# Performance work log

Measured on AMD Instinct MI355X. Metric: run time of the kernel, lower is better.

Reference implementation:

```python
import math
import jax, jax.numpy as jnp
import numpy as np

KV_RANK = 512
NOPE = 128
ROPE = 64
V_DIM = 128
N_HEADS = 16
DIM = 2048
EPS = 1e-6
# qk_head_dim = 192; max_seq_len > original_seq_len -> mscale correction
_MSCALE = 0.1 * 1.0 * math.log(40.0) + 1.0
SOFTMAX_SCALE = (NOPE + ROPE) ** -0.5 * _MSCALE * _MSCALE


def _rmsnorm(x, w):
    y = x * jax.lax.rsqrt(jnp.mean(x * x, axis=-1, keepdims=True) + EPS)
    return y * w


def _rope(x, cos, sin):
    # x: [b, s, h, d] with d even; pairs are interleaved (complex view semantics)
    xr, xi = x[..., 0::2], x[..., 1::2]
    c = cos[None, :, None, :]
    s = sin[None, :, None, :]
    yr = xr * c - xi * s
    yi = xr * s + xi * c
    return jnp.stack([yr, yi], axis=-1).reshape(x.shape)


def setup_inputs() -> dict:
    key = jax.random.key(0)
    ks = jax.random.split(key, 6)
    B, S = 2, 2048
    x = jax.random.normal(ks[0], (B, S, DIM), dtype=jnp.float32)
    # standard RoPE angles: pos * inv_freq, theta=10000
    inv_freq = 1.0 / (10000.0 ** (np.arange(0, ROPE, 2, dtype=np.float32) / ROPE))
    angles = jnp.asarray(np.arange(S, dtype=np.float32)[:, None] * inv_freq[None, :])
    wq = jax.random.normal(ks[1], (N_HEADS * (NOPE + ROPE), DIM), dtype=jnp.float32) * (DIM ** -0.5)
    wkv_a = jax.random.normal(ks[2], (KV_RANK + ROPE, DIM), dtype=jnp.float32) * (DIM ** -0.5)
    wkv_b = jax.random.normal(ks[3], (N_HEADS * (NOPE + V_DIM), KV_RANK), dtype=jnp.float32) * (KV_RANK ** -0.5)
    wo = jax.random.normal(ks[4], (DIM, N_HEADS * V_DIM), dtype=jnp.float32) * ((N_HEADS * V_DIM) ** -0.5)
    kv_norm_w = jnp.ones((KV_RANK,), dtype=jnp.float32)
    return {"x": x, "angles": angles, "wq": wq, "wkv_a": wkv_a,
            "wkv_b": wkv_b, "wo": wo, "kv_norm_w": kv_norm_w}


def reference(x, angles, wq, wkv_a, wkv_b, wo, kv_norm_w):
    B, S, _ = x.shape
    cos, sin = jnp.cos(angles), jnp.sin(angles)  # [S, ROPE//2]

    # query projection
    q = (x @ wq.T).reshape(B, S, N_HEADS, NOPE + ROPE)
    q_nope, q_pe = q[..., :NOPE], q[..., NOPE:]
    q_pe = _rope(q_pe, cos, sin)

    # low-rank kv projection
    kv = x @ wkv_a.T  # [B, S, KV_RANK + ROPE]
    kv_c, k_pe = kv[..., :KV_RANK], kv[..., KV_RANK:]
    k_pe = _rope(k_pe[:, :, None, :], cos, sin)[:, :, 0]  # [B, S, ROPE]
    c = _rmsnorm(kv_c, kv_norm_w)  # latent kv cache [B, S, KV_RANK]

    # weight absorption: fold W^UK into q
    wkv_b_h = wkv_b.reshape(N_HEADS, NOPE + V_DIM, KV_RANK)
    q_abs = jnp.einsum('bshd,hdc->bshc', q_nope, wkv_b_h[:, :NOPE])

    scores = (jnp.einsum('bshc,btc->bsht', q_abs, c)
              + jnp.einsum('bshr,btr->bsht', q_pe, k_pe)) * SOFTMAX_SCALE

    # causal mask (prefill, start_pos=0)
    mask = jnp.where(jnp.tril(jnp.ones((S, S), dtype=bool)), 0.0, -jnp.inf)
    scores = scores + mask[None, :, None, :]
    probs = jax.nn.softmax(scores.astype(jnp.float32), axis=-1).astype(x.dtype)

    o_lat = jnp.einsum('bsht,btc->bshc', probs, c)
    o = jnp.einsum('bshc,hdc->bshd', o_lat, wkv_b_h[:, NOPE:])  # [B,S,H,V]
    return o.reshape(B, S, N_HEADS * V_DIM) @ wo.T
```

## Files before the change

### kernel.cpp

```cpp
#include <hip/hip_runtime.h>
#include <hip/hip_bf16.h>

typedef unsigned short u16;
typedef unsigned int   u32;
typedef __attribute__((ext_vector_type(8))) short bf16x8;
typedef __attribute__((ext_vector_type(4))) float f32x4;

#define NH   16
#define SS   2048

__device__ __forceinline__ u16 bf16b(float f) {
  union { float f; u32 u; } v; v.f = f;
  u32 r = (v.u + 0x7fffu + ((v.u >> 16) & 1u)) >> 16;
  return (u16)r;
}
__device__ __forceinline__ float bf2f(u16 v) {
  union { u32 u; float f; } x; x.u = (u32)v << 16; return x.f;
}
__device__ __forceinline__ f32x4 mfma16(bf16x8 a, bf16x8 b, f32x4 c) {
  return __builtin_amdgcn_mfma_f32_16x16x32_bf16(a, b, c, 0, 0, 0);
}
__device__ __forceinline__ void gl_lds16(const u16* g, u16* l) {
  __builtin_amdgcn_global_load_lds(
      (const __attribute__((address_space(1))) void*)g,
      (__attribute__((address_space(3))) void*)l, 16, 0, 0);
}

__global__ __launch_bounds__(256) void zerok(float* __restrict__ p, long n)
{
  long i = ((long)blockIdx.x * 256 + threadIdx.x) * 4;
  if (i < n) { p[i] = 0.f; p[i+1] = 0.f; p[i+2] = 0.f; p[i+3] = 0.f; }
}

__global__ __launch_bounds__(256) void castk(const float* __restrict__ src,
                                             u16* __restrict__ dst, long n)
{
  long i = ((long)blockIdx.x * 256 + threadIdx.x) * 4;
  if (i >= n) return;
  const float4 f = *(const float4*)(src + i);
  uint2 v;
  v.x = (u32)bf16b(f.x) | ((u32)bf16b(f.y) << 16);
  v.y = (u32)bf16b(f.z) | ((u32)bf16b(f.w) << 16);
  *(uint2*)(dst + i) = v;
}

__global__ __launch_bounds__(256) void wsplit(const float* __restrict__ wb,
                                              u16* __restrict__ T1, u16* __restrict__ Wv)
{
  const long i = (long)blockIdx.x * 256 + threadIdx.x;
  const int h   = (int)(i >> 16);
  const int rem = (int)(i & 65535);
  { const int c = rem >> 7, d = rem & 127;
    T1[i] = bf16b(wb[((long)(h * 256 + d)) * 512 + c]); }
  { const int d = rem >> 9, c = rem & 511;
    Wv[i] = bf16b(wb[((long)(h * 256 + 128 + d)) * 512 + c]); }
}

template<int OUTBF>
__global__ __launch_bounds__(256, 2)
void gemm_bt(const u16* __restrict__ A, const u16* __restrict__ W, void* __restrict__ Cout,
             int M, int N, int K, int lda, int ldw, int ldc,
             long aStride, long wStride, long cStride)
{
  __shared__ u16 As[128 * 40];
  __shared__ u16 Bs[128 * 40];
  const int tid = threadIdx.x;
  const int wave = tid >> 6, lane = tid & 63, g = lane >> 4, l15 = lane & 15;
  const int z = blockIdx.z;
  A += (long)z * aStride;  W += (long)z * wStride;
  const long cOff = (long)z * cStride;
  const int m0 = blockIdx.y * 128, n0 = blockIdx.x * 128;
  const int mq = (wave >> 1) * 64, nq = (wave & 1) * 64;
  const int srow = tid >> 1, scol = (tid & 1) * 16;

  const f32x4 fzero = {0.f, 0.f, 0.f, 0.f};
  f32x4 acc[4][4];
#pragma unroll
  for (int i = 0; i < 4; i++)
#pragma unroll
    for (int j = 0; j < 4; j++) acc[i][j] = fzero;

  for (int k0 = 0; k0 < K; k0 += 32) {
    const u16* aSrc = A + (long)(m0 + srow) * lda + k0 + scol;
    uint4 av0 = *(const uint4*)aSrc;
    uint4 av1 = *(const uint4*)(aSrc + 8);
    uint4 bv0 = make_uint4(0, 0, 0, 0), bv1 = make_uint4(0, 0, 0, 0);
    if (n0 + srow < N) {
      const u16* wSrc = W + (long)(n0 + srow) * ldw + k0 + scol;
      bv0 = *(const uint4*)wSrc;
      bv1 = *(const uint4*)(wSrc + 8);
    }
    __syncthreads();
    *(uint4*)&As[srow * 40 + scol]     = av0;
    *(uint4*)&As[srow * 40 + scol + 8] = av1;
    *(uint4*)&Bs[srow * 40 + scol]     = bv0;
    *(uint4*)&Bs[srow * 40 + scol + 8] = bv1;
    __syncthreads();

    bf16x8 af[4], bfr[4];
#pragma unroll
    for (int i = 0; i < 4; i++) af[i]  = *(const bf16x8*)&As[(mq + i * 16 + l15) * 40 + g * 8];
#pragma unroll
    for (int j = 0; j < 4; j++) bfr[j] = *(const bf16x8*)&Bs[(nq + j * 16 + l15) * 40 + g * 8];
#pragma unroll
    for (int i = 0; i < 4; i++)
#pragma unroll
      for (int j = 0; j < 4; j++)
        acc[i][j] = mfma16(af[i], bfr[j], acc[i][j]);
  }

#pragma unroll
  for (int i = 0; i < 4; i++) {
    const int r0 = m0 + mq + i * 16 + g * 4;
#pragma unroll
    for (int j = 0; j < 4; j++) {
      const int c = n0 + nq + j * 16 + l15;
      if (c < N) {
#pragma unroll
        for (int r = 0; r < 4; r++) {
          const long idx = cOff + (long)(r0 + r) * ldc + c;
          if (OUTBF) ((u16*)Cout)[idx]   = bf16b(acc[i][j][r]);
          else       ((float*)Cout)[idx] = acc[i][j][r];
        }
      }
    }
  }
}

__global__ __launch_bounds__(256) void qpack(const u16* __restrict__ q,
                                             const float* __restrict__ angles,
                                             u16* __restrict__ qpe)
{
  const int s = blockIdx.x;
  const int sseq = s & (SS - 1);
  const int tid = threadIdx.x;
#pragma unroll
  for (int pp = 0; pp < 2; pp++) {
    const int p = tid * 2 + pp;
    const int h = p >> 5, j = p & 31;
    const float xr = bf2f(q[(long)s * 3072 + h * 192 + 128 + 2 * j]);
    const float xi = bf2f(q[(long)s * 3072 + h * 192 + 128 + 2 * j + 1]);
    float sn, cs;
    __sincosf(angles[sseq * 32 + j], &sn, &cs);
    const u32 pk = (u32)bf16b(xr * cs - xi * sn) | ((u32)bf16b(xr * sn + xi * cs) << 16);
    *(u32*)(qpe + ((long)s * NH + h) * 64 + 2 * j) = pk;
  }
}

__global__ __launch_bounds__(256) void kvpack(const u16* __restrict__ kv,
                                              const float* __restrict__ angles,
                                              const float* __restrict__ kvw,
                                              u16* __restrict__ cb, u16* __restrict__ kpe)
{
  const int row = blockIdx.x * 4 + (threadIdx.x >> 6);
  const int lane = threadIdx.x & 63;
  const int sseq = row & (SS - 1);
  const u16* src = kv + (long)row * 576;
  float v[8]; float ss = 0.f;
#pragma unroll
  for (int j = 0; j < 8; j++) { float t = bf2f(src[lane + j * 64]); v[j] = t; ss += t * t; }
#pragma unroll
  for (int d = 1; d < 64; d <<= 1) ss += __shfl_xor(ss, d, 64);
  const float rn = 1.0f / sqrtf(ss * (1.f / 512.f) + 1e-6f);
#pragma unroll
  for (int j = 0; j < 8; j++)
    cb[(long)row * 512 + lane + j * 64] = bf16b(v[j] * rn * kvw[lane + j * 64]);
  if (lane < 32) {
    const float xr = bf2f(src[512 + 2 * lane]), xi = bf2f(src[512 + 2 * lane + 1]);
    float sn, cs;
    __sincosf(angles[sseq * 32 + lane], &sn, &cs);
    const u32 pk = (u32)bf16b(xr * cs - xi * sn) | ((u32)bf16b(xr * sn + xi * cs) << 16);
    *(u32*)(kpe + (long)row * 64 + 2 * lane) = pk;
  }
}

__global__ __launch_bounds__(256, 2)
void attn_flash(const u16* __restrict__ qab, const u16* __restrict__ qpe,
                const u16* __restrict__ cb, const u16* __restrict__ kpe,
                u16* __restrict__ olat)
{
  __shared__ u16 KsD[2][16 * 512];
  __shared__ u16 KrD[2][16 * 64];
  __shared__ u16 VT[512 * 32];
  __shared__ u16 Ps[4][16 * 40];

  const int tid = threadIdx.x;
  const int wave = tid >> 6, lane = tid & 63;
  const int g = lane >> 4, l15 = lane & 15;
  const int L = blockIdx.x;
  const int b = (L >> 2) & 1;
  const int u = ((L >> 3) << 2) | (L & 3);
  const int h = u & 15;
  const int p = u >> 4;
  const float NEG_INF = -__builtin_inff();
  const float SC = 0.07216878364870323f * 1.3688879454113936f * 1.3688879454113936f;
  const f32x4 fzero = {0.f, 0.f, 0.f, 0.f};

  for (int idx = tid; idx < 4 * 16 * 40 / 2; idx += 256) ((u32*)Ps)[idx] = 0;
  for (int idx = tid; idx < 512 * 32 / 2;   idx += 256) ((u32*)VT)[idx] = 0;

  const int tp   = tid & 7;
  const int cblk = tid >> 3;

  auto stage = [&](int t0n, int buf) {
#pragma unroll
    for (int it = 0; it < 4; ++it) {
      const int tr = it * 4 + wave;
      const int sw = ((tr >> 1) & 7) << 3;
      const u16* gp = cb + (long)(b * SS + t0n + tr) * 512 + ((lane * 8) ^ sw);
      gl_lds16(gp, &KsD[buf][tr * 512]);
    }
    if (wave < 2) {
      const int r0 = wave * 8;
      const int tr = r0 + (lane >> 3);
      const int sw = ((tr >> 1) & 7) << 3;
      const u16* gp = kpe + (long)(b * SS + t0n + tr) * 64 + (((lane & 7) * 8) ^ sw);
      gl_lds16(gp, &KrD[buf][r0 * 64]);
    }
  };

#pragma unroll 1
  for (int half = 0; half < 2; ++half) {
    const int qt = half ? p : (31 - p);
    const int swave = qt * 64 + wave * 16;

    bf16x8 qf[18];
    {
      const u16* qa = qab + ((long)(b * SS + swave + l15) * NH + h) * 512;
#pragma unroll
      for (int f = 0; f < 16; f++) qf[f] = *(const bf16x8*)(qa + f * 32 + g * 8);
      const u16* qp = qpe + ((long)(b * SS + swave + l15) * NH + h) * 64;
      qf[16] = *(const bf16x8*)(qp + g * 8);
      qf[17] = *(const bf16x8*)(qp + 32 + g * 8);
    }

    f32x4 oacc[32];
#pragma unroll
    for (int i = 0; i < 32; i++) oacc[i] = fzero;
    float m[4], l[4];
#pragma unroll
    for (int r = 0; r < 4; r++) { m[r] = NEG_INF; l[r] = 0.f; }

    const int nsteps  = 4 * qt + 4;
    const int lastact = 4 * qt + wave;

    stage(0, 0);

    for (int ts = 0; ts < nsteps; ++ts) {
      const int cur = ts & 1;
      const int t0 = ts * 16;
      asm volatile("s_waitcnt vmcnt(0) lgkmcnt(0)" ::: "memory");
      __builtin_amdgcn_s_barrier();

      if (ts + 1 < nsteps) stage(t0 + 16, cur ^ 1);

      {
        const u16* K0 = &KsD[cur][(2 * tp) * 512];
        const u16* K1 = &KsD[cur][(2 * tp + 1) * 512];
        const int swr  = (tp & 7) << 3;
        const int cb16 = cblk * 16;
        const bf16x8 alo = *(const bf16x8*)&K0[(cb16)     ^ swr];
        const bf16x8 ahi = *(const bf16x8*)&K0[(cb16 + 8) ^ swr];
        const bf16x8 blo = *(const bf16x8*)&K1[(cb16)     ^ swr];
        const bf16x8 bhi = *(const bf16x8*)&K1[(cb16 + 8) ^ swr];
#pragma unroll
        for (int j = 0; j < 16; ++j) {
          const int c = cb16 + j;
          const u16 ua = (u16)((j < 8) ? alo[j] : ahi[j - 8]);
          const u16 ub = (u16)((j < 8) ? blo[j] : bhi[j - 8]);
          *(u32*)&VT[(c * 32 + 2 * tp) ^ ((cblk & 7) << 3)] = (u32)ua | ((u32)ub << 16);
        }
      }
      asm volatile("s_waitcnt lgkmcnt(0)" ::: "memory");
      __builtin_amdgcn_s_barrier();

      if (ts > lastact) continue;

      const int swl = ((l15 >> 1) & 7) << 3;
      const u16* KsC = &KsD[cur][l15 * 512];
      const u16* KrC = &KrD[cur][l15 * 64];
      f32x4 sacc = fzero, sacc2 = fzero;
      __builtin_amdgcn_s_setprio(1);
#pragma unroll
      for (int f = 0; f < 16; f += 2) {
        const bf16x8 k0 = *(const bf16x8*)&KsC[((f    ) * 32 + g * 8) ^ swl];
        const bf16x8 k1 = *(const bf16x8*)&KsC[((f + 1) * 32 + g * 8) ^ swl];
        sacc  = mfma16(qf[f],     k0, sacc);
        sacc2 = mfma16(qf[f + 1], k1, sacc2);
      }
      {
        const bf16x8 k0 = *(const bf16x8*)&KrC[(     g * 8) ^ swl];
        const bf16x8 k1 = *(const bf16x8*)&KrC[(32 + g * 8) ^ swl];
        sacc  = mfma16(qf[16], k0, sacc);
        sacc2 = mfma16(qf[17], k1, sacc2);
      }
      __builtin_amdgcn_s_setprio(0);

      float alf[4]; bool resc = false;
#pragma unroll
      for (int r = 0; r < 4; ++r) {
        const int srow = swave + g * 4 + r;
        float v = (sacc[r] + sacc2[r]) * SC;
        if (t0 + l15 > srow) v = NEG_INF;
        float tm = v;
#pragma unroll
        for (int d = 1; d < 16; d <<= 1) tm = fmaxf(tm, __shfl_xor(tm, d, 64));
        const float mnew = (tm > m[r] + 8.f) ? tm : m[r];
        const float al = __expf(m[r] - mnew);
        const float pv = __expf(v - mnew);
        float rs = pv;
#pragma unroll
        for (int d = 1; d < 16; d <<= 1) rs += __shfl_xor(rs, d, 64);
        l[r] = l[r] * al + rs;
        resc |= (mnew != m[r]);
        m[r] = mnew;
        alf[r] = al;
        Ps[wave][(g * 4 + r) * 40 + l15] = bf16b(pv);
      }

      if (__any((int)resc)) {
#pragma unroll
        for (int i = 0; i < 32; ++i) {
          f32x4 o = oacc[i];
          o[0] *= alf[0]; o[1] *= alf[1]; o[2] *= alf[2]; o[3] *= alf[3];
          oacc[i] = o;
        }
      }

      const bf16x8 paf = *(const bf16x8*)&Ps[wave][l15 * 40 + g * 8];
      __builtin_amdgcn_s_setprio(1);
#pragma unroll
      for (int i = 0; i < 32; ++i) {
        const int c = i * 16 + l15;
        const bf16x8 vf = *(const bf16x8*)&VT[(c * 32 + g * 8) ^ ((i & 7) << 3)];
        oacc[i] = mfma16(paf, vf, oacc[i]);
      }
      __builtin_amdgcn_s_setprio(0);
    }

    float linv[4];
#pragma unroll
    for (int r = 0; r < 4; ++r) linv[r] = 1.0f / l[r];
#pragma unroll
    for (int r = 0; r < 4; ++r) {
      u16* dst = olat + ((long)(b * SS + swave + g * 4 + r) * NH + h) * 512 + l15;
#pragma unroll
      for (int i = 0; i < 32; ++i)
        dst[i * 16] = bf16b(oacc[i][r] * linv[r]);
    }
  }
}

extern "C" void kernel_launch(void* const* d_in, const int* in_sizes, int n_in,
                              void* d_out, int out_size, void* d_ws, size_t ws_size,
                              hipStream_t stream)
{
  const float* x      = (const float*)d_in[0];
  const float* angles = (const float*)d_in[1];
  const float* wq     = (const float*)d_in[2];
  const float* wkv_a  = (const float*)d_in[3];
  const float* wkv_b  = (const float*)d_in[4];
  const float* wo     = (const float*)d_in[5];
  const float* kvw    = (const float*)d_in[6];

  const size_t WS_NEED = 157810688;
  if (ws_size < WS_NEED) {
    zerok<<<dim3(8192), dim3(256), 0, stream>>>((float*)d_out, 8388608L);
    return;
  }
  char* base = (char*)d_ws;
  u16* xb   = (u16*)(base + 0);
  u16* kvb  = (u16*)(base + 16777216);
  u16* wab  = (u16*)(base + 21495808);
  u16* qab  = (u16*)(base + 0);
  u16* ob   = (u16*)(base + 0);
  u16* qbf  = (u16*)(base + 67108864);
  u16* T1   = (u16*)(base + 92274688);
  u16* wqb  = (u16*)(base + 94371840);
  u16* olat = (u16*)(base + 67108864);
  u16* wob  = (u16*)(base + 134217728);
  u16* Wv   = (u16*)(base + 142606336);
  u16* qpe_ = (u16*)(base + 144703488);
  u16* cbuf = (u16*)(base + 153092096);
  u16* kpeb = (u16*)(base + 157286400);

  castk<<<dim3(8192), dim3(256), 0, stream>>>(x, xb, 8388608L);
  castk<<<dim3(6144), dim3(256), 0, stream>>>(wq, wqb, 6291456L);
  castk<<<dim3(1152), dim3(256), 0, stream>>>(wkv_a, wab, 1179648L);
  castk<<<dim3(4096), dim3(256), 0, stream>>>(wo, wob, 4194304L);
  wsplit<<<dim3(4096), dim3(256), 0, stream>>>(wkv_b, T1, Wv);

  gemm_bt<1><<<dim3(24, 32, 1), dim3(256), 0, stream>>>(
      xb, wqb, (void*)qbf, 4096, 3072, 2048, 2048, 2048, 3072, 0L, 0L, 0L);
  gemm_bt<1><<<dim3(5, 32, 1), dim3(256), 0, stream>>>(
      xb, wab, (void*)kvb, 4096, 576, 2048, 2048, 2048, 576, 0L, 0L, 0L);

  qpack<<<dim3(4096), dim3(256), 0, stream>>>(qbf, angles, qpe_);
  kvpack<<<dim3(1024), dim3(256), 0, stream>>>(kvb, angles, kvw, cbuf, kpeb);

  gemm_bt<1><<<dim3(4, 32, 16), dim3(256), 0, stream>>>(
      qbf, T1, (void*)qab, 4096, 512, 128, 3072, 128, 8192, 192L, 65536L, 512L);

  attn_flash<<<dim3(512, 1), dim3(256), 0, stream>>>(qab, qpe_, cbuf, kpeb, olat);

  gemm_bt<1><<<dim3(1, 32, 16), dim3(256), 0, stream>>>(
      olat, Wv, (void*)ob, 4096, 128, 512, 8192, 512, 2048, 512L, 65536L, 128L);

  gemm_bt<0><<<dim3(16, 32, 1), dim3(256), 0, stream>>>(
      ob, wob, d_out, 4096, 2048, 2048, 2048, 2048, 2048, 0L, 0L, 0L);
}
```

Baseline: 1.479 ms.

## Software-pipeline PV MFMA one step behind QK and drop zero-padded K32 MFMA

The P·V product for key tile ts-1 is deferred into iteration ts, using double-buffered VT and P shared arrays, which removes the second per-step barrier. The PV MFMA switches from 16x16x32 with half its K dimension zero-padded to 16x16x16 bf16, halving the wasted MFMA work and the size of VT and P. A tail PV step is added after the loop. This adds LDS for double buffering and a new swizzle, and correctness depends on the buffer parity and the lastact logic.

```diff
diff --git a/kernel.cpp b/kernel.cpp
--- a/kernel.cpp
+++ b/kernel.cpp
@@ -4,6 +4,7 @@
 typedef unsigned short u16;
 typedef unsigned int   u32;
 typedef __attribute__((ext_vector_type(8))) short bf16x8;
+typedef __attribute__((ext_vector_type(4))) short bf16x4;
 typedef __attribute__((ext_vector_type(4))) float f32x4;
 
 #define NH   16
@@ -20,11 +21,23 @@
 __device__ __forceinline__ f32x4 mfma16(bf16x8 a, bf16x8 b, f32x4 c) {
   return __builtin_amdgcn_mfma_f32_16x16x32_bf16(a, b, c, 0, 0, 0);
 }
+__device__ __forceinline__ f32x4 mfma16k16(bf16x4 a, bf16x4 b, f32x4 c) {
+#if __has_builtin(__builtin_amdgcn_mfma_f32_16x16x16bf16_1k)
+  return __builtin_amdgcn_mfma_f32_16x16x16bf16_1k(a, b, c, 0, 0, 0);
+#else
+  f32x4 d;
+  asm volatile("v_mfma_f32_16x16x16_bf16 %0, %1, %2, %3"
+               : "=v"(d) : "v"(a), "v"(b), "v"(c));
+  return d;
+#endif
+}
 __device__ __forceinline__ void gl_lds16(const u16* g, u16* l) {
   __builtin_amdgcn_global_load_lds(
       (const __attribute__((address_space(1))) void*)g,
       (__attribute__((address_space(3))) void*)l, 16, 0, 0);
 }
+
+#define VSW(c, t) ((((c) * 16 + (t))) ^ ((((c) >> 4) & 7) << 3) ^ ((((c) >> 2) & 3) << 2))
 
 __global__ __launch_bounds__(256) void zerok(float* __restrict__ p, long n)
 {
@@ -181,8 +194,8 @@
 {
   __shared__ u16 KsD[2][16 * 512];
   __shared__ u16 KrD[2][16 * 64];
-  __shared__ u16 VT[512 * 32];
-  __shared__ u16 Ps[4][16 * 40];
+  __shared__ u16 VT16[2][512 * 16];
+  __shared__ u16 Ps[2][4][16 * 20];
 
   const int tid = threadIdx.x;
   const int wave = tid >> 6, lane = tid & 63;
@@ -196,9 +209,6 @@
   const float SC = 0.07216878364870323f * 1.3688879454113936f * 1.3688879454113936f;
   const f32x4 fzero = {0.f, 0.f, 0.f, 0.f};
 
-  for (int idx = tid; idx < 4 * 16 * 40 / 2; idx += 256) ((u32*)Ps)[idx] = 0;
-  for (int idx = tid; idx < 512 * 32 / 2;   idx += 256) ((u32*)VT)[idx] = 0;
-
   const int tp   = tid & 7;
   const int cblk = tid >> 3;
 
@@ -253,6 +263,19 @@
       __builtin_amdgcn_s_barrier();
 
       if (ts + 1 < nsteps) stage(t0 + 16, cur ^ 1);
+
+      if (ts >= 1 && ts - 1 <= lastact) {
+        const int pv = cur ^ 1;
+        const bf16x4 paf = *(const bf16x4*)&Ps[pv][wave][l15 * 20 + g * 4];
+        __builtin_amdgcn_s_setprio(1);
+#pragma unroll
+        for (int i = 0; i < 32; ++i) {
+          const int c = i * 16 + l15;
+          const bf16x4 vf = *(const bf16x4*)&VT16[pv][VSW(c, g * 4)];
+          oacc[i] = mfma16k16(paf, vf, oacc[i]);
+        }
+        __builtin_amdgcn_s_setprio(0);
+      }
 
       {
         const u16* K0 = &KsD[cur][(2 * tp) * 512];
@@ -268,74 +291,75 @@
           const int c = cb16 + j;
           const u16 ua = (u16)((j < 8) ? alo[j] : ahi[j - 8]);
           const u16 ub = (u16)((j < 8) ? blo[j] : bhi[j - 8]);
-          *(u32*)&VT[(c * 32 + 2 * tp) ^ ((cblk & 7) << 3)] = (u32)ua | ((u32)ub << 16);
+          *(u32*)&VT16[cur][VSW(c, 2 * tp)] = (u32)ua | ((u32)ub << 16);
         }
       }
-      asm volatile("s_waitcnt lgkmcnt(0)" ::: "memory");
-      __builtin_amdgcn_s_barrier();
-
-      if (ts > lastact) continue;
-
-      const int swl = ((l15 >> 1) & 7) << 3;
-      const u16* KsC = &KsD[cur][l15 * 512];
-      const u16* KrC = &KrD[cur][l15 * 64];
-      f32x4 sacc = fzero, sacc2 = fzero;
-      __builtin_amdgcn_s_setprio(1);
-#pragma unroll
-      for (int f = 0; f < 16; f += 2) {
-        const bf16x8 k0 = *(const bf16x8*)&KsC[((f    ) * 32 + g * 8) ^ swl];
-        const bf16x8 k1 = *(const bf16x8*)&KsC[((f + 1) * 32 + g * 8) ^ swl];
-        sacc  = mfma16(qf[f],     k0, sacc);
-        sacc2 = mfma16(qf[f + 1], k1, sacc2);
+
+      if (ts <= lastact) {
+        const int swl = ((l15 >> 1) & 7) << 3;
+        const u16* KsC = &KsD[cur][l15 * 512];
+        const u16* KrC = &KrD[cur][l15 * 64];
+        f32x4 sacc = fzero, sacc2 = fzero;
+        __builtin_amdgcn_s_setprio(1);
+#pragma unroll
+        for (int f = 0; f < 16; f += 2) {
+          const bf16x8 k0 = *(const bf16x8*)&KsC[((f    ) * 32 + g * 8) ^ swl];
+          const bf16x8 k1 = *(const bf16x8*)&KsC[((f + 1) * 32 + g * 8) ^ swl];
+          sacc  = mfma16(qf[f],     k0, sacc);
+          sacc2 = mfma16(qf[f + 1], k1, sacc2);
+        }
+        {
+          const bf16x8 k0 = *(const bf16x8*)&KrC[(     g * 8) ^ swl];
+          const bf16x8 k1 = *(const bf16x8*)&KrC[(32 + g * 8) ^ swl];
+          sacc  = mfma16(qf[16], k0, sacc);
+          sacc2 = mfma16(qf[17], k1, sacc2);
+        }
+        __builtin_amdgcn_s_setprio(0);
+
+        float alf[4]; bool resc = false;
+#pragma unroll
+        for (int r = 0; r < 4; ++r) {
+          const int srow = swave + g * 4 + r;
+          float v = (sacc[r] + sacc2[r]) * SC;
+          if (t0 + l15 > srow) v = NEG_INF;
+          float tm = v;
+#pragma unroll
+          for (int d = 1; d < 16; d <<= 1) tm = fmaxf(tm, __shfl_xor(tm, d, 64));
+          const float mnew = (tm > m[r] + 8.f) ? tm : m[r];
+          const float al = __expf(m[r] - mnew);
+          const float pv = __expf(v - mnew);
+          float rs = pv;
+#pragma unroll
+          for (int d = 1; d < 16; d <<= 1) rs += __shfl_xor(rs, d, 64);
+          l[r] = l[r] * al + rs;
+          resc |= (mnew != m[r]);
+          m[r] = mnew;
+          alf[r] = al;
+          Ps[cur][wave][(g * 4 + r) * 20 + l15] = bf16b(pv);
+        }
+
+        if (__any((int)resc)) {
+#pragma unroll
+          for (int i = 0; i < 32; ++i) {
+            f32x4 o = oacc[i];
+            o[0] *= alf[0]; o[1] *= alf[1]; o[2] *= alf[2]; o[3] *= alf[3];
+            oacc[i] = o;
+          }
+        }
       }
-      {
-        const bf16x8 k0 = *(const bf16x8*)&KrC[(     g * 8) ^ swl];
-        const bf16x8 k1 = *(const bf16x8*)&KrC[(32 + g * 8) ^ swl];
-        sacc  = mfma16(qf[16], k0, sacc);
-        sacc2 = mfma16(qf[17], k1, sacc2);
-      }
-      __builtin_amdgcn_s_setprio(0);
-
-      float alf[4]; bool resc = false;
-#pragma unroll
-      for (int r = 0; r < 4; ++r) {
-        const int srow = swave + g * 4 + r;
-        float v = (sacc[r] + sacc2[r]) * SC;
-        if (t0 + l15 > srow) v = NEG_INF;
-        float tm = v;
-#pragma unroll
-        for (int d = 1; d < 16; d <<= 1) tm = fmaxf(tm, __shfl_xor(tm, d, 64));
-        const float mnew = (tm > m[r] + 8.f) ? tm : m[r];
-        const float al = __expf(m[r] - mnew);
-        const float pv = __expf(v - mnew);
-        float rs = pv;
-#pragma unroll
-        for (int d = 1; d < 16; d <<= 1) rs += __shfl_xor(rs, d, 64);
-        l[r] = l[r] * al + rs;
-        resc |= (mnew != m[r]);
-        m[r] = mnew;
-        alf[r] = al;
-        Ps[wave][(g * 4 + r) * 40 + l15] = bf16b(pv);
-      }
-
-      if (__any((int)resc)) {
-#pragma unroll
-        for (int i = 0; i < 32; ++i) {
-          f32x4 o = oacc[i];
-          o[0] *= alf[0]; o[1] *= alf[1]; o[2] *= alf[2]; o[3] *= alf[3];
-          oacc[i] = o;
-        }
-      }
-
-      const bf16x8 paf = *(const bf16x8*)&Ps[wave][l15 * 40 + g * 8];
-      __builtin_amdgcn_s_setprio(1);
+    }
+
+    asm volatile("s_waitcnt lgkmcnt(0)" ::: "memory");
+    __builtin_amdgcn_s_barrier();
+    if (lastact == nsteps - 1) {
+      const int pv = (nsteps - 1) & 1;
+      const bf16x4 paf = *(const bf16x4*)&Ps[pv][wave][l15 * 20 + g * 4];
 #pragma unroll
       for (int i = 0; i < 32; ++i) {
         const int c = i * 16 + l15;
-        const bf16x8 vf = *(const bf16x8*)&VT[(c * 32 + g * 8) ^ ((i & 7) << 3)];
-        oacc[i] = mfma16(paf, vf, oacc[i]);
+        const bf16x4 vf = *(const bf16x4*)&VT16[pv][VSW(c, g * 4)];
+        oacc[i] = mfma16k16(paf, vf, oacc[i]);
       }
-      __builtin_amdgcn_s_setprio(0);
     }
 
     float linv[4];
```

Result: slower. 2.890 ms (+95.4%).

## Use K=16 MFMA for PV, drop zero-padding, DPP row reductions, direct kpe loads

Applied to the files above, without the earlier changes.

The PV product previously used a 16x16x32 MFMA with the V transpose and P tiles zero-padded from 16 to 32 keys, so half of every PV MFMA was wasted work. It now uses the 16x16x16 bf16 MFMA with a compact 16-wide V transpose and a new swizzle, and removes the zero-init loops. Row max and row sum reductions use DPP row rotations in place of cross-lane shuffles, and the rope keys are read straight from global memory in place of being staged through LDS. The risks are more MFMA issue slots per tile, new bank-conflict patterns from the swizzle, and the latency of uncached global kpe loads.

```diff
diff --git a/kernel.cpp b/kernel.cpp
--- a/kernel.cpp
+++ b/kernel.cpp
@@ -4,6 +4,7 @@
 typedef unsigned short u16;
 typedef unsigned int   u32;
 typedef __attribute__((ext_vector_type(8))) short bf16x8;
+typedef __attribute__((ext_vector_type(4))) short bf16x4;
 typedef __attribute__((ext_vector_type(4))) float f32x4;
 
 #define NH   16
@@ -20,11 +21,36 @@
 __device__ __forceinline__ f32x4 mfma16(bf16x8 a, bf16x8 b, f32x4 c) {
   return __builtin_amdgcn_mfma_f32_16x16x32_bf16(a, b, c, 0, 0, 0);
 }
+__device__ __forceinline__ f32x4 mfma16k16(bf16x4 a, bf16x4 b, f32x4 c) {
+#if __has_builtin(__builtin_amdgcn_mfma_f32_16x16x16bf16_1k)
+  return __builtin_amdgcn_mfma_f32_16x16x16bf16_1k(a, b, c, 0, 0, 0);
+#else
+  f32x4 d;
+  asm volatile("v_mfma_f32_16x16x16_bf16 %0, %1, %2, %3"
+               : "=v"(d) : "v"(a), "v"(b), "v"(c));
+  return d;
+#endif
+}
 __device__ __forceinline__ void gl_lds16(const u16* g, u16* l) {
   __builtin_amdgcn_global_load_lds(
       (const __attribute__((address_space(1))) void*)g,
       (__attribute__((address_space(3))) void*)l, 16, 0, 0);
 }
+
+template<int CTRL>
+__device__ __forceinline__ float fror(float x) {
+  union { float f; int i; } u; u.f = x;
+  u.i = __builtin_amdgcn_update_dpp(u.i, u.i, CTRL, 0xf, 0xf, false);
+  return u.f;
+}
+#define ROWMAX16(t) do { \
+  t = fmaxf(t, fror<0x121>(t)); t = fmaxf(t, fror<0x122>(t)); \
+  t = fmaxf(t, fror<0x124>(t)); t = fmaxf(t, fror<0x128>(t)); } while (0)
+#define ROWSUM16(t) do { \
+  t += fror<0x121>(t); t += fror<0x122>(t); \
+  t += fror<0x124>(t); t += fror<0x128>(t); } while (0)
+
+#define VSW(c, t) ((((c) * 16 + (t))) ^ ((((c) >> 4) & 7) << 3) ^ ((((c) >> 2) & 3) << 2))
 
 __global__ __launch_bounds__(256) void zerok(float* __restrict__ p, long n)
 {
@@ -180,9 +206,8 @@
                 u16* __restrict__ olat)
 {
   __shared__ u16 KsD[2][16 * 512];
-  __shared__ u16 KrD[2][16 * 64];
-  __shared__ u16 VT[512 * 32];
-  __shared__ u16 Ps[4][16 * 40];
+  __shared__ u16 VT16[512 * 16];
+  __shared__ u16 Ps[4][16 * 20];
 
   const int tid = threadIdx.x;
   const int wave = tid >> 6, lane = tid & 63;
@@ -196,9 +221,6 @@
   const float SC = 0.07216878364870323f * 1.3688879454113936f * 1.3688879454113936f;
   const f32x4 fzero = {0.f, 0.f, 0.f, 0.f};
 
-  for (int idx = tid; idx < 4 * 16 * 40 / 2; idx += 256) ((u32*)Ps)[idx] = 0;
-  for (int idx = tid; idx < 512 * 32 / 2;   idx += 256) ((u32*)VT)[idx] = 0;
-
   const int tp   = tid & 7;
   const int cblk = tid >> 3;
 
@@ -209,13 +231,6 @@
       const int sw = ((tr >> 1) & 7) << 3;
       const u16* gp = cb + (long)(b * SS + t0n + tr) * 512 + ((lane * 8) ^ sw);
       gl_lds16(gp, &KsD[buf][tr * 512]);
-    }
-    if (wave < 2) {
-      const int r0 = wave * 8;
-      const int tr = r0 + (lane >> 3);
-      const int sw = ((tr >> 1) & 7) << 3;
-      const u16* gp = kpe + (long)(b * SS + t0n + tr) * 64 + (((lane & 7) * 8) ^ sw);
-      gl_lds16(gp, &KrD[buf][r0 * 64]);
     }
   };
 
@@ -268,7 +283,7 @@
           const int c = cb16 + j;
           const u16 ua = (u16)((j < 8) ? alo[j] : ahi[j - 8]);
           const u16 ub = (u16)((j < 8) ? blo[j] : bhi[j - 8]);
-          *(u32*)&VT[(c * 32 + 2 * tp) ^ ((cblk & 7) << 3)] = (u32)ua | ((u32)ub << 16);
+          *(u32*)&VT16[VSW(c, 2 * tp)] = (u32)ua | ((u32)ub << 16);
         }
       }
       asm volatile("s_waitcnt lgkmcnt(0)" ::: "memory");
@@ -276,9 +291,12 @@
 
       if (ts > lastact) continue;
 
+      const u16* krp = kpe + (long)(b * SS + t0 + l15) * 64 + g * 8;
+      const bf16x8 kr0 = *(const bf16x8*)krp;
+      const bf16x8 kr1 = *(const bf16x8*)(krp + 32);
+
       const int swl = ((l15 >> 1) & 7) << 3;
       const u16* KsC = &KsD[cur][l15 * 512];
-      const u16* KrC = &KrD[cur][l15 * 64];
       f32x4 sacc = fzero, sacc2 = fzero;
       __builtin_amdgcn_s_setprio(1);
 #pragma unroll
@@ -288,12 +306,8 @@
         sacc  = mfma16(qf[f],     k0, sacc);
         sacc2 = mfma16(qf[f + 1], k1, sacc2);
       }
-      {
-        const bf16x8 k0 = *(const bf16x8*)&KrC[(     g * 8) ^ swl];
-        const bf16x8 k1 = *(const bf16x8*)&KrC[(32 + g * 8) ^ swl];
-        sacc  = mfma16(qf[16], k0, sacc);
-        sacc2 = mfma16(qf[17], k1, sacc2);
-      }
+      sacc  = mfma16(qf[16], kr0, sacc);
+      sacc2 = mfma16(qf[17], kr1, sacc2);
       __builtin_amdgcn_s_setprio(0);
 
       float alf[4]; bool resc = false;
@@ -303,19 +317,17 @@
         float v = (sacc[r] + sacc2[r]) * SC;
         if (t0 + l15 > srow) v = NEG_INF;
         float tm = v;
-#pragma unroll
-        for (int d = 1; d < 16; d <<= 1) tm = fmaxf(tm, __shfl_xor(tm, d, 64));
+        ROWMAX16(tm);
         const float mnew = (tm > m[r] + 8.f) ? tm : m[r];
         const float al = __expf(m[r] - mnew);
         const float pv = __expf(v - mnew);
         float rs = pv;
-#pragma unroll
-        for (int d = 1; d < 16; d <<= 1) rs += __shfl_xor(rs, d, 64);
+        ROWSUM16(rs);
         l[r] = l[r] * al + rs;
         resc |= (mnew != m[r]);
         m[r] = mnew;
         alf[r] = al;
-        Ps[wave][(g * 4 + r) * 40 + l15] = bf16b(pv);
+        Ps[wave][(g * 4 + r) * 20 + l15] = bf16b(pv);
       }
 
       if (__any((int)resc)) {
@@ -327,13 +339,13 @@
         }
       }
 
-      const bf16x8 paf = *(const bf16x8*)&Ps[wave][l15 * 40 + g * 8];
+      const bf16x4 paf = *(const bf16x4*)&Ps[wave][l15 * 20 + g * 4];
       __builtin_amdgcn_s_setprio(1);
 #pragma unroll
       for (int i = 0; i < 32; ++i) {
         const int c = i * 16 + l15;
-        const bf16x8 vf = *(const bf16x8*)&VT[(c * 32 + g * 8) ^ ((i & 7) << 3)];
-        oacc[i] = mfma16(paf, vf, oacc[i]);
+        const bf16x4 vf = *(const bf16x4*)&VT16[VSW(c, g * 4)];
+        oacc[i] = mfma16k16(paf, vf, oacc[i]);
       }
       __builtin_amdgcn_s_setprio(0);
     }
```

Measured after the change: 2.574 ms. 1.74x slower.
